# Performance work log

Measured on AMD Instinct MI355X. Metric: run time of the kernel, lower is better.

Reference implementation:

```python
import jax, jax.numpy as jnp
import numpy as np

IN_C, OUT_C, MX, MY = 64, 64, 32, 32
B, H, W = 16, 256, 256


def setup_inputs() -> dict:
    key = jax.random.key(0)
    k1, k2, k3 = jax.random.split(key, 3)
    scale = 1.0 / (IN_C * OUT_C)
    x = jax.random.normal(k1, (B, IN_C, H, W), dtype=jnp.float32)
    weight_real = scale * jax.random.normal(k2, (IN_C, OUT_C, MX, MY), dtype=jnp.float32)
    weight_imag = scale * jax.random.normal(k3, (IN_C, OUT_C, MX, MY), dtype=jnp.float32)
    return {"x": x, "weight_real": weight_real, "weight_imag": weight_imag}


def reference(x, weight_real, weight_imag):
    Bv, C, Hv, Wv = x.shape
    x_ft = jnp.fft.rfft2(x, norm="ortho")  # [B, C_in, H, W//2+1] complex64
    mx = min(MX, Hv)
    my = min(MY, Wv // 2 + 1)
    x_crop = x_ft[:, :, :mx, :my]
    w = (weight_real[:, :, :mx, :my] + 1j * weight_imag[:, :, :mx, :my]).astype(jnp.complex64)
    # complex contraction over in_channels: [B,i,x,y] x [i,o,x,y] -> [B,o,x,y]
    out_modes = jnp.einsum("bixy,ioxy->boxy", x_crop, w)
    out_ft = jnp.zeros((Bv, OUT_C, Hv, Wv // 2 + 1), dtype=jnp.complex64)
    out_ft = out_ft.at[:, :, :mx, :my].set(out_modes)
    return jnp.fft.irfft2(out_ft, s=(Hv, Wv), norm="ortho")
```

## Files before the change

### kernel.cpp

```cpp
#include <hip/hip_runtime.h>
#include <math.h>


__global__ __launch_bounds__(256) void k_tables(float* __restrict__ ws) {
    int idx = blockIdx.x * 256 + threadIdx.x;
    const float STEP = 6.283185307179586f / 256.f;
    float s, c;
    {
        int w = idx >> 5, ky = idx & 31;
        int t = (w * ky) & 255;
        sincosf((float)t * STEP, &s, &c);
        ws[w * 64 + 2 * ky]     = c * (1.f / 256.f);
        ws[w * 64 + 2 * ky + 1] = -s * (1.f / 256.f);
    }
    {
        int kx = idx >> 8, h = idx & 255;
        int t = (kx * h) & 255;
        sincosf((float)t * STEP, &s, &c);
        ((float2*)(ws + 16384))[kx * 256 + h] = make_float2(c, s);
    }
    {
        int ky = idx >> 8, w = idx & 255;
        int t = (ky * w) & 255;
        sincosf((float)t * STEP, &s, &c);
        float cc = (ky == 0 ? 1.f : 2.f) / 256.f;
        ws[32768 + (2 * ky) * 256 + w]     = cc * c;
        ws[32768 + (2 * ky + 1) * 256 + w] = -cc * s;
    }
}

__global__ __launch_bounds__(256) void k_f1(const float* __restrict__ x,
                                            const float* __restrict__ e1,
                                            float* __restrict__ y) {
    __shared__ float As[32 * 132];
    __shared__ float Bs[32 * 64];
    int t = threadIdx.x, tx = t & 15, ty = t >> 4;
    int row0 = blockIdx.x * 128;
    float acc[8][4];
#pragma unroll
    for (int i = 0; i < 8; ++i)
#pragma unroll
        for (int j = 0; j < 4; ++j) acc[i][j] = 0.f;

    for (int kt = 0; kt < 8; ++kt) {
#pragma unroll
        for (int n = 0; n < 4; ++n) {
            int f4 = t + n * 256;
            int r = f4 >> 3, c4 = f4 & 7;
            float4 v = *(const float4*)&x[(long)(row0 + r) * 256 + kt * 32 + c4 * 4];
            As[(c4 * 4 + 0) * 132 + r] = v.x;
            As[(c4 * 4 + 1) * 132 + r] = v.y;
            As[(c4 * 4 + 2) * 132 + r] = v.z;
            As[(c4 * 4 + 3) * 132 + r] = v.w;
        }
#pragma unroll
        for (int n = 0; n < 2; ++n) {
            int f4 = t + n * 256;
            int k = f4 >> 4, c4 = f4 & 15;
            *(float4*)&Bs[k * 64 + c4 * 4] = *(const float4*)&e1[(kt * 32 + k) * 64 + c4 * 4];
        }
        __syncthreads();
#pragma unroll
        for (int k = 0; k < 32; ++k) {
            float4 a0 = *(const float4*)&As[k * 132 + ty * 4];
            float4 a1 = *(const float4*)&As[k * 132 + 64 + ty * 4];
            float4 b0 = *(const float4*)&Bs[k * 64 + tx * 4];
            float av[8] = {a0.x, a0.y, a0.z, a0.w, a1.x, a1.y, a1.z, a1.w};
            float bv[4] = {b0.x, b0.y, b0.z, b0.w};
#pragma unroll
            for (int i = 0; i < 8; ++i)
#pragma unroll
                for (int j = 0; j < 4; ++j)
                    acc[i][j] = fmaf(av[i], bv[j], acc[i][j]);
        }
        __syncthreads();
    }
#pragma unroll
    for (int i = 0; i < 8; ++i) {
        int r = row0 + ((i < 4) ? (ty * 4 + i) : (64 + ty * 4 + i - 4));
        float4 v = make_float4(acc[i][0], acc[i][1], acc[i][2], acc[i][3]);
        *(float4*)&y[(long)r * 64 + tx * 4] = v;
    }
}

__global__ __launch_bounds__(256) void k_f2(const float2* __restrict__ tt,
                                            const float2* __restrict__ y,
                                            float2* __restrict__ xf) {
    __shared__ float smem[2176 + 2048];
    float* As = smem;
    float* Bs = smem + 2176;
    int t = threadIdx.x, tx = t & 15, ty = t >> 4;
    int batch = blockIdx.x;
    const float2* ybase = y + (long)batch * 256 * 32;
    float acc[4][4];
#pragma unroll
    for (int i = 0; i < 4; ++i)
#pragma unroll
        for (int j = 0; j < 4; ++j) acc[i][j] = 0.f;

    for (int ht = 0; ht < 8; ++ht) {
        int h0 = ht * 32;
#pragma unroll
        for (int n = 0; n < 4; ++n) {
            int i2 = t + n * 256;
            int kx = i2 >> 5, hh = i2 & 31;
            float2 cs = tt[kx * 256 + h0 + hh];
            As[hh * 68 + kx] = cs.x;
            As[hh * 68 + 32 + kx] = cs.y;
        }
#pragma unroll
        for (int n = 0; n < 4; ++n) {
            int i2 = t + n * 256;
            int hh = i2 >> 5, ky = i2 & 31;
            float2 v = ybase[(h0 + hh) * 32 + ky];
            *(float2*)&Bs[hh * 64 + 2 * ky] = v;
        }
        __syncthreads();
#pragma unroll
        for (int kk = 0; kk < 32; ++kk) {
            float4 a0 = *(const float4*)&As[kk * 68 + ty * 4];
            float4 b0 = *(const float4*)&Bs[kk * 64 + tx * 4];
            float av[4] = {a0.x, a0.y, a0.z, a0.w};
            float bv[4] = {b0.x, b0.y, b0.z, b0.w};
#pragma unroll
            for (int i = 0; i < 4; ++i)
#pragma unroll
                for (int j = 0; j < 4; ++j)
                    acc[i][j] = fmaf(av[i], bv[j], acc[i][j]);
        }
        __syncthreads();
    }
    float* Cs = smem;
#pragma unroll
    for (int i = 0; i < 4; ++i)
#pragma unroll
        for (int j = 0; j < 4; ++j)
            Cs[(ty * 4 + i) * 65 + tx * 4 + j] = acc[i][j];
    __syncthreads();
#pragma unroll
    for (int n = 0; n < 4; ++n) {
        int idx = t + n * 256;
        int kx = idx >> 5, ky = idx & 31;
        float re = Cs[kx * 65 + 2 * ky]     + Cs[(kx + 32) * 65 + 2 * ky + 1];
        float im = Cs[kx * 65 + 2 * ky + 1] - Cs[(kx + 32) * 65 + 2 * ky];
        xf[(long)batch * 1024 + kx * 32 + ky] = make_float2(re, im);
    }
}

__global__ __launch_bounds__(256) void k_mix(const float* __restrict__ wr,
                                             const float* __restrict__ wi,
                                             const float2* __restrict__ xf,
                                             float2* __restrict__ om) {
    __shared__ float2 xs[64 * 32];
    int t = threadIdx.x;
    int b = blockIdx.x >> 5, kx = blockIdx.x & 31;
#pragma unroll
    for (int n = 0; n < 8; ++n) {
        int i2 = t + n * 256;
        int i = i2 >> 5, ky = i2 & 31;
        xs[i2] = xf[(long)(b * 64 + i) * 1024 + kx * 32 + ky];
    }
    __syncthreads();
    int ky = t & 31, og = t >> 5;
    float ar[8], ai[8];
#pragma unroll
    for (int j = 0; j < 8; ++j) { ar[j] = 0.f; ai[j] = 0.f; }
    const float* wrb = wr + kx * 32 + ky;
    const float* wib = wi + kx * 32 + ky;
    for (int i = 0; i < 64; ++i) {
        float2 xv = xs[i * 32 + ky];
#pragma unroll
        for (int j = 0; j < 8; ++j) {
            int o = og * 8 + j;
            long woff = (long)(i * 64 + o) * 1024;
            float wrv = wrb[woff], wiv = wib[woff];
            ar[j] = fmaf(xv.x, wrv, fmaf(-xv.y, wiv, ar[j]));
            ai[j] = fmaf(xv.x, wiv, fmaf(xv.y, wrv, ai[j]));
        }
    }
    float2* omb = om + (long)(b * 64) * 1024 + kx * 32 + ky;
#pragma unroll
    for (int j = 0; j < 8; ++j) {
        int o = og * 8 + j;
        omb[(long)o * 1024] = make_float2(ar[j], ai[j]);
    }
}

__global__ __launch_bounds__(256) void k_i1(const float2* __restrict__ tt,
                                            const float2* __restrict__ om,
                                            float2* __restrict__ g) {
    __shared__ float As[64 * 68];
    __shared__ float Bs[64 * 64];
    int t = threadIdx.x, tx = t & 15, ty = t >> 4;
    int bo = blockIdx.x >> 2, hb = blockIdx.x & 3;
    int h0 = hb * 64;
#pragma unroll
    for (int n = 0; n < 8; ++n) {
        int i2 = t + n * 256;
        int kx = i2 >> 6, hh = i2 & 63;
        float2 cs = tt[kx * 256 + h0 + hh];
        As[kx * 68 + hh] = cs.x;
        As[(kx + 32) * 68 + hh] = cs.y;
    }
    const float2* ombase = om + (long)bo * 1024;
#pragma unroll
    for (int n = 0; n < 4; ++n) {
        int i2 = t + n * 256;
        int kx = i2 >> 5, ky = i2 & 31;
        float2 v = ombase[kx * 32 + ky];
        Bs[kx * 64 + 2 * ky] = v.x;
        Bs[kx * 64 + 2 * ky + 1] = v.y;
        Bs[(kx + 32) * 64 + 2 * ky] = -v.y;
        Bs[(kx + 32) * 64 + 2 * ky + 1] = v.x;
    }
    __syncthreads();
    float acc[4][4];
#pragma unroll
    for (int i = 0; i < 4; ++i)
#pragma unroll
        for (int j = 0; j < 4; ++j) acc[i][j] = 0.f;
#pragma unroll 16
    for (int k = 0; k < 64; ++k) {
        float4 a0 = *(const float4*)&As[k * 68 + ty * 4];
        float4 b0 = *(const float4*)&Bs[k * 64 + tx * 4];
        float av[4] = {a0.x, a0.y, a0.z, a0.w};
        float bv[4] = {b0.x, b0.y, b0.z, b0.w};
#pragma unroll
        for (int i = 0; i < 4; ++i)
#pragma unroll
            for (int j = 0; j < 4; ++j)
                acc[i][j] = fmaf(av[i], bv[j], acc[i][j]);
    }
    float2* gbase = g + (long)bo * 256 * 32;
#pragma unroll
    for (int i = 0; i < 4; ++i) {
        float4 v = make_float4(acc[i][0], acc[i][1], acc[i][2], acc[i][3]);
        *(float4*)&gbase[(h0 + ty * 4 + i) * 32 + tx * 2] = v;
    }
}

__global__ __launch_bounds__(256) void k_i2(const float* __restrict__ g,
                                            const float* __restrict__ e2,
                                            float* __restrict__ out) {
    __shared__ float As[64 * 68];
    __shared__ float Bs[64 * 128];
    int t = threadIdx.x, tx = t & 15, ty = t >> 4;
    int rb = blockIdx.x >> 1, wb = blockIdx.x & 1;
    int row0 = rb * 64;
#pragma unroll
    for (int n = 0; n < 4; ++n) {
        int f4 = t + n * 256;
        int r = f4 >> 4, c4 = f4 & 15;
        float4 v = *(const float4*)&g[(long)(row0 + r) * 64 + c4 * 4];
        As[(c4 * 4 + 0) * 68 + r] = v.x;
        As[(c4 * 4 + 1) * 68 + r] = v.y;
        As[(c4 * 4 + 2) * 68 + r] = v.z;
        As[(c4 * 4 + 3) * 68 + r] = v.w;
    }
#pragma unroll
    for (int n = 0; n < 8; ++n) {
        int f4 = t + n * 256;
        int k = f4 >> 5, w4 = f4 & 31;
        *(float4*)&Bs[k * 128 + w4 * 4] = *(const float4*)&e2[k * 256 + wb * 128 + w4 * 4];
    }
    __syncthreads();
    float acc[4][8];
#pragma unroll
    for (int i = 0; i < 4; ++i)
#pragma unroll
        for (int j = 0; j < 8; ++j) acc[i][j] = 0.f;
#pragma unroll 16
    for (int k = 0; k < 64; ++k) {
        float4 a0 = *(const float4*)&As[k * 68 + ty * 4];
        float4 b0 = *(const float4*)&Bs[k * 128 + tx * 4];
        float4 b1 = *(const float4*)&Bs[k * 128 + 64 + tx * 4];
        float av[4] = {a0.x, a0.y, a0.z, a0.w};
        float bv[8] = {b0.x, b0.y, b0.z, b0.w, b1.x, b1.y, b1.z, b1.w};
#pragma unroll
        for (int i = 0; i < 4; ++i)
#pragma unroll
            for (int j = 0; j < 8; ++j)
                acc[i][j] = fmaf(av[i], bv[j], acc[i][j]);
    }
#pragma unroll
    for (int i = 0; i < 4; ++i) {
        long ro = (long)(row0 + ty * 4 + i) * 256 + wb * 128;
        float4 v0 = make_float4(acc[i][0], acc[i][1], acc[i][2], acc[i][3]);
        float4 v1 = make_float4(acc[i][4], acc[i][5], acc[i][6], acc[i][7]);
        *(float4*)&out[ro + tx * 4] = v0;
        *(float4*)&out[ro + 64 + tx * 4] = v1;
    }
}

extern "C" void kernel_launch(void* const* d_in, const int* in_sizes, int n_in,
                              void* d_out, int out_size, void* d_ws, size_t ws_size,
                              hipStream_t stream) {
    const float* x  = (const float*)d_in[0];
    const float* wr = (const float*)d_in[1];
    const float* wi = (const float*)d_in[2];
    float* out = (float*)d_out;
    float* ws = (float*)d_ws;

    float*  e1 = ws;
    float2* tt = (float2*)(ws + 16384);
    float*  e2 = ws + 32768;
    float*  y  = ws + 65536;
    float*  xf = ws + 65536 + 16777216;
    float*  om = ws + 65536 + 16777216 + 2097152;
    float*  g  = y;

    hipLaunchKernelGGL(k_tables, dim3(32),   dim3(256), 0, stream, ws);
    hipLaunchKernelGGL(k_f1,     dim3(2048), dim3(256), 0, stream, x, e1, y);
    hipLaunchKernelGGL(k_f2,     dim3(1024), dim3(256), 0, stream, tt, (const float2*)y, (float2*)xf);
    hipLaunchKernelGGL(k_mix,    dim3(512),  dim3(256), 0, stream, wr, wi, (const float2*)xf, (float2*)om);
    hipLaunchKernelGGL(k_i1,     dim3(4096), dim3(256), 0, stream, tt, (const float2*)om, (float2*)g);
    hipLaunchKernelGGL(k_i2,     dim3(8192), dim3(256), 0, stream, g, e2, out);
}
```

Measured before the change: 688.3 us.

## Run DFT GEMMs on MFMA with split-fp16 hi/lo emulation of fp32

```diff
diff --git a/kernel.cpp b/kernel.cpp
--- a/kernel.cpp
+++ b/kernel.cpp
@@ -1,86 +1,116 @@
 #include <hip/hip_runtime.h>
 #include <math.h>
 
+
+typedef _Float16 f16x4 __attribute__((ext_vector_type(4)));
+typedef _Float16 f16x8 __attribute__((ext_vector_type(8)));
+typedef float f32x4 __attribute__((ext_vector_type(4)));
 
 __global__ __launch_bounds__(256) void k_tables(float* __restrict__ ws) {
     int idx = blockIdx.x * 256 + threadIdx.x;
     const float STEP = 6.283185307179586f / 256.f;
     float s, c;
     {
-        int w = idx >> 5, ky = idx & 31;
-        int t = (w * ky) & 255;
-        sincosf((float)t * STEP, &s, &c);
-        ws[w * 64 + 2 * ky]     = c * (1.f / 256.f);
-        ws[w * 64 + 2 * ky + 1] = -s * (1.f / 256.f);
-    }
-    {
         int kx = idx >> 8, h = idx & 255;
         int t = (kx * h) & 255;
         sincosf((float)t * STEP, &s, &c);
         ((float2*)(ws + 16384))[kx * 256 + h] = make_float2(c, s);
     }
-    {
-        int ky = idx >> 8, w = idx & 255;
-        int t = (ky * w) & 255;
-        sincosf((float)t * STEP, &s, &c);
-        float cc = (ky == 0 ? 1.f : 2.f) / 256.f;
-        ws[32768 + (2 * ky) * 256 + w]     = cc * c;
-        ws[32768 + (2 * ky + 1) * 256 + w] = -cc * s;
+    _Float16* e1h = (_Float16*)ws;
+    _Float16* e1l = (_Float16*)(ws + 8192);
+    _Float16* e2h = (_Float16*)(ws + 32768);
+    _Float16* e2l = (_Float16*)(ws + 40960);
+    if (idx < 2048) {
+        int l = idx & 63, nt = (idx >> 6) & 3, kt = idx >> 8;
+        int col = nt * 16 + (l & 15);
+        int ky = col >> 1;
+        int kb = kt * 32 + (l >> 4) * 8;
+#pragma unroll
+        for (int j = 0; j < 8; ++j) {
+            int k = kb + j;
+            int tt_ = (k * ky) & 255;
+            sincosf((float)tt_ * STEP, &s, &c);
+            float val = ((col & 1) ? -s : c) * 256.f;
+            _Float16 h = (_Float16)val;
+            e1h[idx * 8 + j] = h;
+            e1l[idx * 8 + j] = (_Float16)(val - (float)h);
+        }
+    } else if (idx < 4096) {
+        int i2 = idx - 2048;
+        int l = i2 & 63, nt = (i2 >> 6) & 15, kt = i2 >> 10;
+        int w = nt * 16 + (l & 15);
+        int kb = kt * 32 + (l >> 4) * 8;
+#pragma unroll
+        for (int j = 0; j < 8; ++j) {
+            int k = kb + j;
+            int ky = k >> 1;
+            int tt_ = (ky * w) & 255;
+            sincosf((float)tt_ * STEP, &s, &c);
+            float val = ((k & 1) ? -s : c) * 256.f;
+            _Float16 h = (_Float16)val;
+            e2h[i2 * 8 + j] = h;
+            e2l[i2 * 8 + j] = (_Float16)(val - (float)h);
+        }
     }
 }
 
 __global__ __launch_bounds__(256) void k_f1(const float* __restrict__ x,
-                                            const float* __restrict__ e1,
+                                            const _Float16* __restrict__ e1h,
+                                            const _Float16* __restrict__ e1l,
                                             float* __restrict__ y) {
-    __shared__ float As[32 * 132];
-    __shared__ float Bs[32 * 64];
-    int t = threadIdx.x, tx = t & 15, ty = t >> 4;
-    int row0 = blockIdx.x * 128;
-    float acc[8][4];
-#pragma unroll
-    for (int i = 0; i < 8; ++i)
-#pragma unroll
-        for (int j = 0; j < 4; ++j) acc[i][j] = 0.f;
+    __shared__ _Float16 Ah[128 * 40];
+    __shared__ _Float16 Al[128 * 40];
+    int t = threadIdx.x, lane = t & 63, wv = t >> 6;
+    long row0 = (long)blockIdx.x * 128;
+    f32x4 acc[2][4];
+#pragma unroll
+    for (int m = 0; m < 2; ++m)
+#pragma unroll
+        for (int n = 0; n < 4; ++n) acc[m][n] = (f32x4){0.f, 0.f, 0.f, 0.f};
+    int abase = (wv * 32 + (lane & 15)) * 40 + (lane >> 4) * 8;
 
     for (int kt = 0; kt < 8; ++kt) {
 #pragma unroll
         for (int n = 0; n < 4; ++n) {
             int f4 = t + n * 256;
             int r = f4 >> 3, c4 = f4 & 7;
-            float4 v = *(const float4*)&x[(long)(row0 + r) * 256 + kt * 32 + c4 * 4];
-            As[(c4 * 4 + 0) * 132 + r] = v.x;
-            As[(c4 * 4 + 1) * 132 + r] = v.y;
-            As[(c4 * 4 + 2) * 132 + r] = v.z;
-            As[(c4 * 4 + 3) * 132 + r] = v.w;
-        }
-#pragma unroll
-        for (int n = 0; n < 2; ++n) {
-            int f4 = t + n * 256;
-            int k = f4 >> 4, c4 = f4 & 15;
-            *(float4*)&Bs[k * 64 + c4 * 4] = *(const float4*)&e1[(kt * 32 + k) * 64 + c4 * 4];
+            float4 v = *(const float4*)&x[(row0 + r) * 256 + kt * 32 + c4 * 4];
+            float s0 = v.x * 256.f, s1 = v.y * 256.f, s2 = v.z * 256.f, s3 = v.w * 256.f;
+            _Float16 h0 = (_Float16)s0, h1 = (_Float16)s1;
+            _Float16 h2 = (_Float16)s2, h3 = (_Float16)s3;
+            *(f16x4*)&Ah[r * 40 + c4 * 4] = (f16x4){h0, h1, h2, h3};
+            *(f16x4*)&Al[r * 40 + c4 * 4] =
+                (f16x4){(_Float16)(s0 - (float)h0), (_Float16)(s1 - (float)h1),
+                        (_Float16)(s2 - (float)h2), (_Float16)(s3 - (float)h3)};
         }
         __syncthreads();
-#pragma unroll
-        for (int k = 0; k < 32; ++k) {
-            float4 a0 = *(const float4*)&As[k * 132 + ty * 4];
-            float4 a1 = *(const float4*)&As[k * 132 + 64 + ty * 4];
-            float4 b0 = *(const float4*)&Bs[k * 64 + tx * 4];
-            float av[8] = {a0.x, a0.y, a0.z, a0.w, a1.x, a1.y, a1.z, a1.w};
-            float bv[4] = {b0.x, b0.y, b0.z, b0.w};
-#pragma unroll
-            for (int i = 0; i < 8; ++i)
-#pragma unroll
-                for (int j = 0; j < 4; ++j)
-                    acc[i][j] = fmaf(av[i], bv[j], acc[i][j]);
+        f16x8 ah0 = *(const f16x8*)&Ah[abase];
+        f16x8 ah1 = *(const f16x8*)&Ah[abase + 16 * 40];
+        f16x8 al0 = *(const f16x8*)&Al[abase];
+        f16x8 al1 = *(const f16x8*)&Al[abase + 16 * 40];
+#pragma unroll
+        for (int n = 0; n < 4; ++n) {
+            f16x8 bh = *(const f16x8*)(e1h + ((kt * 4 + n) * 64 + lane) * 8);
+            f16x8 bl = *(const f16x8*)(e1l + ((kt * 4 + n) * 64 + lane) * 8);
+            acc[0][n] = __builtin_amdgcn_mfma_f32_16x16x32_f16(ah0, bh, acc[0][n], 0, 0, 0);
+            acc[0][n] = __builtin_amdgcn_mfma_f32_16x16x32_f16(al0, bh, acc[0][n], 0, 0, 0);
+            acc[0][n] = __builtin_amdgcn_mfma_f32_16x16x32_f16(ah0, bl, acc[0][n], 0, 0, 0);
+            acc[1][n] = __builtin_amdgcn_mfma_f32_16x16x32_f16(ah1, bh, acc[1][n], 0, 0, 0);
+            acc[1][n] = __builtin_amdgcn_mfma_f32_16x16x32_f16(al1, bh, acc[1][n], 0, 0, 0);
+            acc[1][n] = __builtin_amdgcn_mfma_f32_16x16x32_f16(ah1, bl, acc[1][n], 0, 0, 0);
         }
         __syncthreads();
     }
-#pragma unroll
-    for (int i = 0; i < 8; ++i) {
-        int r = row0 + ((i < 4) ? (ty * 4 + i) : (64 + ty * 4 + i - 4));
-        float4 v = make_float4(acc[i][0], acc[i][1], acc[i][2], acc[i][3]);
-        *(float4*)&y[(long)r * 64 + tx * 4] = v;
-    }
+    const float SC = 1.f / 16777216.f;
+#pragma unroll
+    for (int m = 0; m < 2; ++m)
+#pragma unroll
+        for (int n = 0; n < 4; ++n)
+#pragma unroll
+            for (int r = 0; r < 4; ++r) {
+                long row = row0 + wv * 32 + m * 16 + (lane >> 4) * 4 + r;
+                y[row * 64 + n * 16 + (lane & 15)] = acc[m][n][r] * SC;
+            }
 }
 
 __global__ __launch_bounds__(256) void k_f2(const float2* __restrict__ tt,
@@ -232,64 +262,71 @@
                 acc[i][j] = fmaf(av[i], bv[j], acc[i][j]);
     }
     float2* gbase = g + (long)bo * 256 * 32;
+    float sa = (tx == 0) ? 1.f : 2.f;
 #pragma unroll
     for (int i = 0; i < 4; ++i) {
-        float4 v = make_float4(acc[i][0], acc[i][1], acc[i][2], acc[i][3]);
+        float4 v = make_float4(acc[i][0] * sa, acc[i][1] * sa, acc[i][2] * 2.f, acc[i][3] * 2.f);
         *(float4*)&gbase[(h0 + ty * 4 + i) * 32 + tx * 2] = v;
     }
 }
 
 __global__ __launch_bounds__(256) void k_i2(const float* __restrict__ g,
-                                            const float* __restrict__ e2,
+                                            const _Float16* __restrict__ e2h,
+                                            const _Float16* __restrict__ e2l,
                                             float* __restrict__ out) {
-    __shared__ float As[64 * 68];
-    __shared__ float Bs[64 * 128];
-    int t = threadIdx.x, tx = t & 15, ty = t >> 4;
-    int rb = blockIdx.x >> 1, wb = blockIdx.x & 1;
-    int row0 = rb * 64;
-#pragma unroll
-    for (int n = 0; n < 4; ++n) {
+    __shared__ _Float16 Ah[32 * 72];
+    __shared__ _Float16 Al[32 * 72];
+    int t = threadIdx.x, lane = t & 63, wv = t >> 6;
+    long row0 = (long)blockIdx.x * 32;
+#pragma unroll
+    for (int n = 0; n < 2; ++n) {
         int f4 = t + n * 256;
         int r = f4 >> 4, c4 = f4 & 15;
-        float4 v = *(const float4*)&g[(long)(row0 + r) * 64 + c4 * 4];
-        As[(c4 * 4 + 0) * 68 + r] = v.x;
-        As[(c4 * 4 + 1) * 68 + r] = v.y;
-        As[(c4 * 4 + 2) * 68 + r] = v.z;
-        As[(c4 * 4 + 3) * 68 + r] = v.w;
-    }
-#pragma unroll
-    for (int n = 0; n < 8; ++n) {
-        int f4 = t + n * 256;
-        int k = f4 >> 5, w4 = f4 & 31;
-        *(float4*)&Bs[k * 128 + w4 * 4] = *(const float4*)&e2[k * 256 + wb * 128 + w4 * 4];
+        float4 v = *(const float4*)&g[(row0 + r) * 64 + c4 * 4];
+        float s0 = v.x * 256.f, s1 = v.y * 256.f, s2 = v.z * 256.f, s3 = v.w * 256.f;
+        _Float16 h0 = (_Float16)s0, h1 = (_Float16)s1;
+        _Float16 h2 = (_Float16)s2, h3 = (_Float16)s3;
+        *(f16x4*)&Ah[r * 72 + c4 * 4] = (f16x4){h0, h1, h2, h3};
+        *(f16x4*)&Al[r * 72 + c4 * 4] =
+            (f16x4){(_Float16)(s0 - (float)h0), (_Float16)(s1 - (float)h1),
+                    (_Float16)(s2 - (float)h2), (_Float16)(s3 - (float)h3)};
     }
     __syncthreads();
-    float acc[4][8];
-#pragma unroll
-    for (int i = 0; i < 4; ++i)
-#pragma unroll
-        for (int j = 0; j < 8; ++j) acc[i][j] = 0.f;
-#pragma unroll 16
-    for (int k = 0; k < 64; ++k) {
-        float4 a0 = *(const float4*)&As[k * 68 + ty * 4];
-        float4 b0 = *(const float4*)&Bs[k * 128 + tx * 4];
-        float4 b1 = *(const float4*)&Bs[k * 128 + 64 + tx * 4];
-        float av[4] = {a0.x, a0.y, a0.z, a0.w};
-        float bv[8] = {b0.x, b0.y, b0.z, b0.w, b1.x, b1.y, b1.z, b1.w};
-#pragma unroll
-        for (int i = 0; i < 4; ++i)
-#pragma unroll
-            for (int j = 0; j < 8; ++j)
-                acc[i][j] = fmaf(av[i], bv[j], acc[i][j]);
-    }
-#pragma unroll
-    for (int i = 0; i < 4; ++i) {
-        long ro = (long)(row0 + ty * 4 + i) * 256 + wb * 128;
-        float4 v0 = make_float4(acc[i][0], acc[i][1], acc[i][2], acc[i][3]);
-        float4 v1 = make_float4(acc[i][4], acc[i][5], acc[i][6], acc[i][7]);
-        *(float4*)&out[ro + tx * 4] = v0;
-        *(float4*)&out[ro + 64 + tx * 4] = v1;
-    }
+    f32x4 acc[2][4];
+#pragma unroll
+    for (int m = 0; m < 2; ++m)
+#pragma unroll
+        for (int n = 0; n < 4; ++n) acc[m][n] = (f32x4){0.f, 0.f, 0.f, 0.f};
+#pragma unroll
+    for (int kt = 0; kt < 2; ++kt) {
+        int abase = (lane & 15) * 72 + kt * 32 + (lane >> 4) * 8;
+        f16x8 ah0 = *(const f16x8*)&Ah[abase];
+        f16x8 ah1 = *(const f16x8*)&Ah[abase + 16 * 72];
+        f16x8 al0 = *(const f16x8*)&Al[abase];
+        f16x8 al1 = *(const f16x8*)&Al[abase + 16 * 72];
+#pragma unroll
+        for (int n = 0; n < 4; ++n) {
+            int nb = ((kt * 16 + wv * 4 + n) * 64 + lane) * 8;
+            f16x8 bh = *(const f16x8*)(e2h + nb);
+            f16x8 bl = *(const f16x8*)(e2l + nb);
+            acc[0][n] = __builtin_amdgcn_mfma_f32_16x16x32_f16(ah0, bh, acc[0][n], 0, 0, 0);
+            acc[0][n] = __builtin_amdgcn_mfma_f32_16x16x32_f16(al0, bh, acc[0][n], 0, 0, 0);
+            acc[0][n] = __builtin_amdgcn_mfma_f32_16x16x32_f16(ah0, bl, acc[0][n], 0, 0, 0);
+            acc[1][n] = __builtin_amdgcn_mfma_f32_16x16x32_f16(ah1, bh, acc[1][n], 0, 0, 0);
+            acc[1][n] = __builtin_amdgcn_mfma_f32_16x16x32_f16(al1, bh, acc[1][n], 0, 0, 0);
+            acc[1][n] = __builtin_amdgcn_mfma_f32_16x16x32_f16(ah1, bl, acc[1][n], 0, 0, 0);
+        }
+    }
+    const float SC = 1.f / 16777216.f;
+#pragma unroll
+    for (int m = 0; m < 2; ++m)
+#pragma unroll
+        for (int n = 0; n < 4; ++n)
+#pragma unroll
+            for (int r = 0; r < 4; ++r) {
+                long row = row0 + m * 16 + (lane >> 4) * 4 + r;
+                out[row * 256 + wv * 64 + n * 16 + (lane & 15)] = acc[m][n][r] * SC;
+            }
 }
 
 extern "C" void kernel_launch(void* const* d_in, const int* in_sizes, int n_in,
@@ -301,18 +338,20 @@
     float* out = (float*)d_out;
     float* ws = (float*)d_ws;
 
-    float*  e1 = ws;
+    const _Float16* e1h = (const _Float16*)ws;
+    const _Float16* e1l = (const _Float16*)(ws + 8192);
     float2* tt = (float2*)(ws + 16384);
-    float*  e2 = ws + 32768;
-    float*  y  = ws + 65536;
-    float*  xf = ws + 65536 + 16777216;
-    float*  om = ws + 65536 + 16777216 + 2097152;
-    float*  g  = y;
+    const _Float16* e2h = (const _Float16*)(ws + 32768);
+    const _Float16* e2l = (const _Float16*)(ws + 40960);
+    float* y  = ws + 65536;
+    float* xf = ws + 65536 + 16777216;
+    float* om = ws + 65536 + 16777216 + 2097152;
+    float* g  = y;
 
     hipLaunchKernelGGL(k_tables, dim3(32),   dim3(256), 0, stream, ws);
-    hipLaunchKernelGGL(k_f1,     dim3(2048), dim3(256), 0, stream, x, e1, y);
+    hipLaunchKernelGGL(k_f1,     dim3(2048), dim3(256), 0, stream, x, e1h, e1l, y);
     hipLaunchKernelGGL(k_f2,     dim3(1024), dim3(256), 0, stream, tt, (const float2*)y, (float2*)xf);
     hipLaunchKernelGGL(k_mix,    dim3(512),  dim3(256), 0, stream, wr, wi, (const float2*)xf, (float2*)om);
     hipLaunchKernelGGL(k_i1,     dim3(4096), dim3(256), 0, stream, tt, (const float2*)om, (float2*)g);
-    hipLaunchKernelGGL(k_i2,     dim3(8192), dim3(256), 0, stream, g, e2, out);
-}
+    hipLaunchKernelGGL(k_i2,     dim3(8192), dim3(256), 0, stream, g, e2h, e2l, out);
+}
```

Measured after the change: 613.0 us. 1.12x faster.
